# Kernel optimization log

Hardware: AMD Instinct MI355X
Metric: run time of the kernel (lower is better)

Reference implementation:

```python
import jax, jax.numpy as jnp
import numpy as np

NUM_HEADS = 16
HEAD_DIM = 64
D_MODEL = 1024
WINDOW = 256
ROPE_BASE = 10000.0
LN_EPS = 1e-5


def setup_inputs() -> dict:
    key = jax.random.key(0)
    k1, k2, k3, k4 = jax.random.split(key, 4)
    B, S, D = 1, 2048, D_MODEL
    x = jax.random.normal(k1, (B, S, D), dtype=jnp.float32)
    state = jax.random.normal(k2, (B, D), dtype=jnp.float32)
    # nn.Linear(d, 3d, bias=False): y = x @ W_qkv with W_qkv: [D, 3D]
    W_qkv = jax.random.normal(k3, (D, 3 * D), dtype=jnp.float32) / np.sqrt(D)
    W_out = jax.random.normal(k4, (D, D), dtype=jnp.float32) / np.sqrt(D)
    ln_gamma = jnp.ones((D,), dtype=jnp.float32)
    ln_beta = jnp.zeros((D,), dtype=jnp.float32)
    return {"x": x, "state": state, "W_qkv": W_qkv, "W_out": W_out,
            "ln_gamma": ln_gamma, "ln_beta": ln_beta}


def _rotate_half(t):
    h = t.shape[-1] // 2
    return jnp.concatenate([-t[..., h:], t[..., :h]], axis=-1)


def _rope(q, k):
    # q, k: [B, H, S, Hd]
    S, Hd = q.shape[2], q.shape[3]
    inv_freq = 1.0 / (ROPE_BASE ** (jnp.arange(0, Hd, 2, dtype=jnp.float32) / Hd))
    ang = jnp.arange(S, dtype=jnp.float32)[:, None] * inv_freq[None, :]  # [S, Hd/2]
    cos = jnp.concatenate([jnp.cos(ang), jnp.cos(ang)], axis=-1)[None, None]  # [1,1,S,Hd]
    sin = jnp.concatenate([jnp.sin(ang), jnp.sin(ang)], axis=-1)[None, None]
    return q * cos + _rotate_half(q) * sin, k * cos + _rotate_half(k) * sin


def _local_causal_mask(S):
    idx = jnp.arange(S)
    dist = idx[:, None] - idx[None, :]
    allowed = (dist >= 0) & (dist <= WINDOW)
    # Faithful to source: allowed positions get 1.0 (softmax-shift-invariant), else -inf
    return jnp.where(allowed, 1.0, -jnp.inf).astype(jnp.float32)[None, None]


def reference(x, state, W_qkv, W_out, ln_gamma, ln_beta):
    B, S, D = x.shape
    H, Hd = NUM_HEADS, HEAD_DIM
    qkv = (x @ W_qkv).reshape(B, S, 3, H, Hd).transpose(2, 0, 3, 1, 4)  # [3,B,H,S,Hd]
    q, k, v = qkv[0], qkv[1], qkv[2]
    q, k = _rope(q, k)
    scores = jnp.einsum("bhsd,bhtd->bhst", q, k) / np.sqrt(Hd) + _local_causal_mask(S)
    attn = jax.nn.softmax(scores, axis=-1)
    out = jnp.einsum("bhst,bhtd->bhsd", attn, v)  # [B,H,S,Hd]
    out = out.transpose(0, 2, 1, 3).reshape(B, S, D)
    res = x + out @ W_out
    mu = jnp.mean(res, axis=-1, keepdims=True)
    var = jnp.var(res, axis=-1, keepdims=True)
    y = (res - mu) * jax.lax.rsqrt(var + LN_EPS) * ln_gamma + ln_beta
    return y, state
```

## Files before the change

### kernel.cpp

```cpp
#include <hip/hip_runtime.h>
#include <math.h>

#define S_LEN 2048
#define DMODEL 1024
#define NHEADS 16
#define HDIM 64
#define WIN 256
#define N_QKV 3072

typedef __attribute__((ext_vector_type(8))) short s16x8;
typedef __attribute__((ext_vector_type(8))) _Float16 f16x8;
typedef __attribute__((ext_vector_type(4))) _Float16 f16x4;
typedef __attribute__((ext_vector_type(4))) float f32x4;

__device__ inline unsigned short f2bf(float f) {
    unsigned int u = __float_as_uint(f);
    u += 0x7FFFu + ((u >> 16) & 1u);
    return (unsigned short)(u >> 16);
}
__device__ inline float bf2f(unsigned short h) {
    return __uint_as_float(((unsigned int)h) << 16);
}

__global__ __launch_bounds__(256) void cvt_f16(
    const float* __restrict__ src, _Float16* __restrict__ dst)
{
    int i = blockIdx.x * 256 + threadIdx.x;
    float4 v = *(const float4*)&src[i * 4];
    f16x4 o;
    o[0] = (_Float16)v.x; o[1] = (_Float16)v.y;
    o[2] = (_Float16)v.z; o[3] = (_Float16)v.w;
    *(f16x4*)&dst[i * 4] = o;
}

__global__ __launch_bounds__(256) void transpose_cvt(
    const float* __restrict__ W, _Float16* __restrict__ T, int K, int N)
{
    __shared__ float t[32][33];
    const int tx = threadIdx.x & 31;
    const int ty = threadIdx.x >> 5;
    const int n0 = blockIdx.x * 32, k0 = blockIdx.y * 32;

    #pragma unroll
    for (int i = 0; i < 4; ++i)
        t[ty + i * 8][tx] = W[(size_t)(k0 + ty + i * 8) * N + n0 + tx];
    __syncthreads();
    #pragma unroll
    for (int i = 0; i < 4; ++i) {
        int n = n0 + ty + i * 8;
        T[(size_t)n * K + k0 + tx] = (_Float16)t[tx][ty + i * 8];
    }
}

template<int BM, int BN, int WM, int WN, bool RES>
__global__ __launch_bounds__(256) void gemm_f16(
    const _Float16* __restrict__ A, const _Float16* __restrict__ B,
    const float* __restrict__ resid, float* __restrict__ C,
    int M, int N, int K)
{
    constexpr int MI = WM / 16;
    constexpr int NJ = WN / 16;
    constexpr int APASS = BM / 64;
    constexpr int BPASS = BN / 64;
    static_assert(WM * 2 == BM && WN * 2 == BN, "4 waves as 2x2");

    __shared__ _Float16 As[BM * 32];
    __shared__ _Float16 Bs[BN * 32];

    const int tid  = threadIdx.x;
    const int w    = tid >> 6;
    const int lane = tid & 63;
    const int m16  = lane & 15;
    const int g    = lane >> 4;
    const int wr   = w >> 1, wc = w & 1;
    const int bm   = blockIdx.y * BM, bn = blockIdx.x * BN;

    f32x4 acc[MI][NJ];
    #pragma unroll
    for (int i = 0; i < MI; ++i)
        #pragma unroll
        for (int j = 0; j < NJ; ++j) acc[i][j] = (f32x4)(0.0f);

    uint4 ra[APASS], rb[BPASS];

    #pragma unroll
    for (int p = 0; p < APASS; ++p) {
        int f = p * 256 + tid, row = f >> 2, cb = f & 3;
        ra[p] = *(const uint4*)&A[(size_t)(bm + row) * K + cb * 8];
    }
    #pragma unroll
    for (int p = 0; p < BPASS; ++p) {
        int f = p * 256 + tid, row = f >> 2, cb = f & 3;
        rb[p] = *(const uint4*)&B[(size_t)(bn + row) * K + cb * 8];
    }

    const int NT = K / 32;
    for (int kt = 0; kt < NT; ++kt) {
        __syncthreads();
        #pragma unroll
        for (int p = 0; p < APASS; ++p) {
            int f = p * 256 + tid, row = f >> 2, cb = f & 3;
            *(uint4*)&As[row * 32 + ((cb ^ ((row >> 1) & 3)) << 3)] = ra[p];
        }
        #pragma unroll
        for (int p = 0; p < BPASS; ++p) {
            int f = p * 256 + tid, row = f >> 2, cb = f & 3;
            *(uint4*)&Bs[row * 32 + ((cb ^ ((row >> 1) & 3)) << 3)] = rb[p];
        }
        __syncthreads();

        if (kt + 1 < NT) {
            int k0 = (kt + 1) * 32;
            #pragma unroll
            for (int p = 0; p < APASS; ++p) {
                int f = p * 256 + tid, row = f >> 2, cb = f & 3;
                ra[p] = *(const uint4*)&A[(size_t)(bm + row) * K + k0 + cb * 8];
            }
            #pragma unroll
            for (int p = 0; p < BPASS; ++p) {
                int f = p * 256 + tid, row = f >> 2, cb = f & 3;
                rb[p] = *(const uint4*)&B[(size_t)(bn + row) * K + k0 + cb * 8];
            }
        }

        f16x8 af[MI], bf_[NJ];
        #pragma unroll
        for (int i = 0; i < MI; ++i) {
            int row = wr * WM + i * 16 + m16;
            af[i] = *(const f16x8*)&As[row * 32 + ((g ^ ((row >> 1) & 3)) << 3)];
        }
        #pragma unroll
        for (int j = 0; j < NJ; ++j) {
            int row = wc * WN + j * 16 + m16;
            bf_[j] = *(const f16x8*)&Bs[row * 32 + ((g ^ ((row >> 1) & 3)) << 3)];
        }
        #pragma unroll
        for (int j = 0; j < NJ; ++j)
            #pragma unroll
            for (int i = 0; i < MI; ++i)
                acc[i][j] = __builtin_amdgcn_mfma_f32_16x16x32_f16(
                    af[i], bf_[j], acc[i][j], 0, 0, 0);
    }

    const int g4 = g * 4;
    #pragma unroll
    for (int i = 0; i < MI; ++i)
        #pragma unroll
        for (int j = 0; j < NJ; ++j) {
            int col = bn + wc * WN + j * 16 + m16;
            #pragma unroll
            for (int r = 0; r < 4; ++r) {
                int row = bm + wr * WM + i * 16 + g4 + r;
                float val = acc[i][j][r];
                if (RES) val += resid[(size_t)row * N + col];
                C[(size_t)row * N + col] = val;
            }
        }
}

__global__ __launch_bounds__(256) void rope_scatter(
    const float* __restrict__ qkv, float* __restrict__ q,
    unsigned short* __restrict__ khi, unsigned short* __restrict__ klo)
{
    int idx = blockIdx.x * 256 + threadIdx.x;
    int s  = idx >> 10;
    int r  = idx & 1023;
    int hd = r & 63;
    int h  = r >> 6;
    const float* row = qkv + (size_t)s * N_QKV;

    float qv = row[r];
    float kv = row[DMODEL + r];

    int   i   = hd & 31;
    float inv = expf(-(float)i * 0.2878231366242553f);
    float ang = (float)s * inv;
    float c  = cosf(ang);
    float sn = sinf(ang);

    int   pr  = (hd < 32) ? r + 32 : r - 32;
    float sgn = (hd < 32) ? -1.0f : 1.0f;

    float qo = qv * c + sgn * row[pr] * sn;
    float ko = kv * c + sgn * row[DMODEL + pr] * sn;

    size_t o = ((size_t)h * S_LEN + s) * HDIM + hd;
    q[o] = qo;
    unsigned short kh = f2bf(ko);
    khi[o] = kh;
    klo[o] = f2bf(ko - bf2f(kh));
}

__global__ __launch_bounds__(256) void v_transpose(
    const float* __restrict__ qkv, unsigned short* __restrict__ vT)
{
    __shared__ float t[64][65];
    const int s0 = blockIdx.x * 64;
    const int h  = blockIdx.y;
    const int tid = threadIdx.x;
    const int dq  = (tid & 15) * 4;
    const int sl0 = tid >> 4;

    #pragma unroll
    for (int p = 0; p < 4; ++p) {
        int sl = sl0 + p * 16;
        float4 v = *(const float4*)&qkv[(size_t)(s0 + sl) * N_QKV + 2 * DMODEL + h * HDIM + dq];
        t[sl][dq] = v.x; t[sl][dq + 1] = v.y; t[sl][dq + 2] = v.z; t[sl][dq + 3] = v.w;
    }
    __syncthreads();
    #pragma unroll
    for (int p = 0; p < 2; ++p) {
        int u = tid + p * 256;
        int d = u >> 3, sb = (u & 7) * 8;
        s16x8 o;
        #pragma unroll
        for (int i = 0; i < 8; ++i) o[i] = (short)f2bf(t[sb + i][d]);
        *(s16x8*)&vT[((size_t)h * HDIM + d) * S_LEN + s0 + sb] = o;
    }
}

#define KP 72
__global__ __launch_bounds__(256, 3) void attn_mfma(
    const float* __restrict__ qg, const unsigned short* __restrict__ khg,
    const unsigned short* __restrict__ klg, const unsigned short* __restrict__ vTg,
    _Float16* __restrict__ oh)
{
    __shared__ __align__(16) unsigned short Kh[64][KP], Kl[64][KP], Vt[64][KP];
    __shared__ __align__(16) unsigned short Pw[4][16][40];

    const int h   = blockIdx.y;
    const int s0  = blockIdx.x * 64;
    const int tid = threadIdx.x;
    const int w   = tid >> 6, lane = tid & 63;
    const int m16 = lane & 15, g = lane >> 4;
    const int t_base = s0 - 256;

    const int qrow = s0 + w * 16 + m16;
    const float* qp = qg + ((size_t)h * S_LEN + qrow) * HDIM;
    s16x8 qh[2], ql[2];
    #pragma unroll
    for (int c = 0; c < 2; ++c) {
        float4 f0 = *(const float4*)&qp[c * 32 + g * 8];
        float4 f1 = *(const float4*)&qp[c * 32 + g * 8 + 4];
        float f[8] = {f0.x, f0.y, f0.z, f0.w, f1.x, f1.y, f1.z, f1.w};
        #pragma unroll
        for (int j = 0; j < 8; ++j) {
            float v = f[j] * 0.125f;
            unsigned short hb = f2bf(v);
            qh[c][j] = (short)hb;
            ql[c][j] = (short)f2bf(v - bf2f(hb));
        }
    }

    const int qb = w * 16 + m16;
    int lo_b = 256 - s0; if (lo_b < qb) lo_b = qb;
    const int hi_b = qb + 256;

    f32x4 O[4];
    #pragma unroll
    for (int nt = 0; nt < 4; ++nt) O[nt] = (f32x4)(0.0f);
    float l_r[4] = {0.0f, 0.0f, 0.0f, 0.0f};
    float m_col = -1e30f;

    const int stage_min = (s0 >= 256) ? 0 : ((193 - s0 + 63) >> 6);

    for (int st = stage_min; st < 5; ++st) {
        __syncthreads();
        const int t0s = t_base + st * 64;
        #pragma unroll
        for (int pp = 0; pp < 2; ++pp) {
            int u = tid + pp * 256;
            int row = u >> 3, cb = (u & 7) * 8;
            int t = t0s + row;
            s16x8 vh = {}, vl = {};
            if (t >= 0) {
                size_t base = ((size_t)h * S_LEN + t) * HDIM + cb;
                vh = *(const s16x8*)&khg[base];
                vl = *(const s16x8*)&klg[base];
            }
            *(s16x8*)&Kh[row][cb] = vh;
            *(s16x8*)&Kl[row][cb] = vl;
        }
        #pragma unroll
        for (int pp = 0; pp < 2; ++pp) {
            int u = tid + pp * 256;
            int d = u >> 3, kb = (u & 7) * 8;
            int t = t0s + kb;
            s16x8 vv = {};
            if (t >= 0)
                vv = *(const s16x8*)&vTg[((size_t)h * HDIM + d) * S_LEN + t];
            *(s16x8*)&Vt[d][kb] = vv;
        }
        __syncthreads();

        #pragma unroll
        for (int ch = 0; ch < 2; ++ch) {
            f32x4 sc[2];
            #pragma unroll
            for (int kt2 = 0; kt2 < 2; ++kt2) {
                int krow = ch * 32 + kt2 * 16 + m16;
                s16x8 kh0 = *(const s16x8*)&Kh[krow][g * 8];
                s16x8 kh1 = *(const s16x8*)&Kh[krow][32 + g * 8];
                s16x8 kl0 = *(const s16x8*)&Kl[krow][g * 8];
                s16x8 kl1 = *(const s16x8*)&Kl[krow][32 + g * 8];
                f32x4 a = (f32x4)(0.0f);
                a = __builtin_amdgcn_mfma_f32_16x16x32_bf16(kh0, qh[0], a, 0, 0, 0);
                a = __builtin_amdgcn_mfma_f32_16x16x32_bf16(kh1, qh[1], a, 0, 0, 0);
                a = __builtin_amdgcn_mfma_f32_16x16x32_bf16(kh0, ql[0], a, 0, 0, 0);
                a = __builtin_amdgcn_mfma_f32_16x16x32_bf16(kh1, ql[1], a, 0, 0, 0);
                a = __builtin_amdgcn_mfma_f32_16x16x32_bf16(kl0, qh[0], a, 0, 0, 0);
                a = __builtin_amdgcn_mfma_f32_16x16x32_bf16(kl1, qh[1], a, 0, 0, 0);
                sc[kt2] = a;
            }

            float scm[8];
            float pmax = -1e30f;
            #pragma unroll
            for (int kt2 = 0; kt2 < 2; ++kt2)
                #pragma unroll
                for (int r = 0; r < 4; ++r) {
                    int ki = st * 64 + ch * 32 + kt2 * 16 + 4 * g + r;
                    bool vd = (ki >= lo_b) && (ki <= hi_b);
                    float s_ = vd ? sc[kt2][r] : -1e30f;
                    scm[kt2 * 4 + r] = s_;
                    pmax = fmaxf(pmax, s_);
                }
            pmax = fmaxf(pmax, __shfl_xor(pmax, 16));
            pmax = fmaxf(pmax, __shfl_xor(pmax, 32));
            float mnew = fmaxf(m_col, pmax);

            float p[8];
            float psum = 0.0f;
            #pragma unroll
            for (int i = 0; i < 8; ++i) {
                float e = (scm[i] > -9e29f) ? __expf(scm[i] - mnew) : 0.0f;
                p[i] = e;
                psum += e;
            }
            psum += __shfl_xor(psum, 16);
            psum += __shfl_xor(psum, 32);
            float scale = __expf(m_col - mnew);
            m_col = mnew;

            #pragma unroll
            for (int r = 0; r < 4; ++r) {
                float sr = __shfl(scale, 4 * g + r);
                float ps = __shfl(psum, 4 * g + r);
                l_r[r] = l_r[r] * sr + ps;
                O[0][r] *= sr; O[1][r] *= sr; O[2][r] *= sr; O[3][r] *= sr;
            }

            unsigned int d0, d1, d2, d3;
            asm("v_cvt_pk_bf16_f32 %0, %1, %2" : "=v"(d0) : "v"(p[0]), "v"(p[1]));
            asm("v_cvt_pk_bf16_f32 %0, %1, %2" : "=v"(d1) : "v"(p[2]), "v"(p[3]));
            asm("v_cvt_pk_bf16_f32 %0, %1, %2" : "=v"(d2) : "v"(p[4]), "v"(p[5]));
            asm("v_cvt_pk_bf16_f32 %0, %1, %2" : "=v"(d3) : "v"(p[6]), "v"(p[7]));
            *(uint2*)&Pw[w][m16][4 * g]      = make_uint2(d0, d1);
            *(uint2*)&Pw[w][m16][16 + 4 * g] = make_uint2(d2, d3);
            asm volatile("s_waitcnt lgkmcnt(0)" ::: "memory");
            __builtin_amdgcn_sched_barrier(0);
            s16x8 pa = *(const s16x8*)&Pw[w][m16][g * 8];

            #pragma unroll
            for (int nt = 0; nt < 4; ++nt) {
                s16x8 vb = *(const s16x8*)&Vt[nt * 16 + m16][ch * 32 + g * 8];
                O[nt] = __builtin_amdgcn_mfma_f32_16x16x32_bf16(pa, vb, O[nt], 0, 0, 0);
            }
        }
    }

    #pragma unroll
    for (int r = 0; r < 4; ++r) {
        float linv = 1.0f / l_r[r];
        int srow = s0 + w * 16 + 4 * g + r;
        size_t obase = (size_t)srow * DMODEL + h * HDIM;
        #pragma unroll
        for (int nt = 0; nt < 4; ++nt)
            oh[obase + nt * 16 + m16] = (_Float16)(O[nt][r] * linv);
    }
}

__global__ __launch_bounds__(256) void layernorm_k(
    const float* __restrict__ res, const float* __restrict__ gamma,
    const float* __restrict__ beta, float* __restrict__ y)
{
    const int row  = blockIdx.x;
    const int tid  = threadIdx.x;
    const int wave = tid >> 6;
    const int lane = tid & 63;
    const float* r = res + (size_t)row * DMODEL;

    float4 xv = *(const float4*)&r[tid * 4];
    float ssum = xv.x + xv.y + xv.z + xv.w;
    float ssq  = xv.x * xv.x + xv.y * xv.y + xv.z * xv.z + xv.w * xv.w;

    #pragma unroll
    for (int off = 1; off < 64; off <<= 1) {
        ssum += __shfl_xor(ssum, off);
        ssq  += __shfl_xor(ssq, off);
    }

    __shared__ float wsum[4], wsq[4];
    if (lane == 0) { wsum[wave] = ssum; wsq[wave] = ssq; }
    __syncthreads();

    float tot  = wsum[0] + wsum[1] + wsum[2] + wsum[3];
    float tot2 = wsq[0] + wsq[1] + wsq[2] + wsq[3];
    float mu   = tot * (1.0f / DMODEL);
    float var  = tot2 * (1.0f / DMODEL) - mu * mu;
    float rstd = rsqrtf(var + 1e-5f);

    float4 gm = *(const float4*)&gamma[tid * 4];
    float4 be = *(const float4*)&beta[tid * 4];
    float4 yo;
    yo.x = (xv.x - mu) * rstd * gm.x + be.x;
    yo.y = (xv.y - mu) * rstd * gm.y + be.y;
    yo.z = (xv.z - mu) * rstd * gm.z + be.z;
    yo.w = (xv.w - mu) * rstd * gm.w + be.w;
    *(float4*)&y[(size_t)row * DMODEL + tid * 4] = yo;
}

extern "C" void kernel_launch(void* const* d_in, const int* in_sizes, int n_in,
                              void* d_out, int out_size, void* d_ws, size_t ws_size,
                              hipStream_t stream) {
    const float* x     = (const float*)d_in[0];
    const float* state = (const float*)d_in[1];
    const float* Wqkv  = (const float*)d_in[2];
    const float* Wout  = (const float*)d_in[3];
    const float* gamma = (const float*)d_in[4];
    const float* beta  = (const float*)d_in[5];
    float* out = (float*)d_out;

    char* base = (char*)d_ws;
    float*     qkv_raw = (float*)base;
    _Float16*  ah      = (_Float16*)base;
    float*     res     = (float*)(base + 8388608);
    float*          qb  = (float*)(base + 25165824);
    unsigned short* khi = (unsigned short*)(base + 33554432);
    unsigned short* klo = (unsigned short*)(base + 37748736);
    unsigned short* vT  = (unsigned short*)(base + 41943040);
    _Float16* WqkvT = (_Float16*)(base + 46137344);
    _Float16* WoutT = (_Float16*)(base + 52428800);
    _Float16* xh    = (_Float16*)(base + 54525952);

    cvt_f16<<<(S_LEN * DMODEL) / 1024, 256, 0, stream>>>(x, xh);
    transpose_cvt<<<dim3(N_QKV / 32, DMODEL / 32), 256, 0, stream>>>(
        Wqkv, WqkvT, DMODEL, N_QKV);
    transpose_cvt<<<dim3(DMODEL / 32, DMODEL / 32), 256, 0, stream>>>(
        Wout, WoutT, DMODEL, DMODEL);

    gemm_f16<128, 64, 64, 32, false>
        <<<dim3(N_QKV / 64, S_LEN / 128), 256, 0, stream>>>(
            xh, WqkvT, nullptr, qkv_raw, S_LEN, N_QKV, DMODEL);

    rope_scatter<<<(S_LEN * DMODEL) / 256, 256, 0, stream>>>(qkv_raw, qb, khi, klo);

    v_transpose<<<dim3(S_LEN / 64, NHEADS), 256, 0, stream>>>(qkv_raw, vT);

    attn_mfma<<<dim3(S_LEN / 64, NHEADS), 256, 0, stream>>>(
        qb, khi, klo, vT, ah);

    gemm_f16<64, 64, 32, 32, true>
        <<<dim3(DMODEL / 64, S_LEN / 64), 256, 0, stream>>>(
            ah, WoutT, x, res, S_LEN, DMODEL, DMODEL);

    layernorm_k<<<S_LEN, 256, 0, stream>>>(res, gamma, beta, out);

    hipMemcpyAsync(out + (size_t)S_LEN * DMODEL, state,
                   (size_t)DMODEL * sizeof(float),
                   hipMemcpyDeviceToDevice, stream);
}
```

Baseline: 185.1 us.

## Use fp16 single-pass QK, direct-to-LDS GEMM loads, precomputed RoPE table

Replaces the split-bf16 (hi/lo) three-term QK^T product with a single fp16 MFMA pass, folding the 1/sqrt(d) scale into RoPE and storing q and k as fp16. The GEMMs switch from register-staged double buffering to global_load_lds direct loads with a new swizzle, and the QKV GEMM tile grows to 128x128. RoPE cos/sin values are precomputed into a table by a separate kernel instead of being evaluated per element. These changes cut QK MFMA work, memory traffic and transcendental math. The costs are reduced precision in the scores and the loss of prefetch overlap in the GEMM main loop.

```diff
diff --git a/kernel.cpp b/kernel.cpp
--- a/kernel.cpp
+++ b/kernel.cpp
@@ -13,6 +13,9 @@
 typedef __attribute__((ext_vector_type(4))) _Float16 f16x4;
 typedef __attribute__((ext_vector_type(4))) float f32x4;
 
+typedef __attribute__((address_space(1))) const void gas_void;
+typedef __attribute__((address_space(3))) void las_void;
+
 __device__ inline unsigned short f2bf(float f) {
     unsigned int u = __float_as_uint(f);
     u += 0x7FFFu + ((u >> 16) & 1u);
@@ -33,6 +36,15 @@
     *(f16x4*)&dst[i * 4] = o;
 }
 
+__global__ __launch_bounds__(256) void rope_tab_k(float2* __restrict__ tab)
+{
+    int idx = blockIdx.x * 256 + threadIdx.x;
+    int s = idx >> 5, i = idx & 31;
+    float inv = expf(-(float)i * 0.2878231366242553f);
+    float ang = (float)s * inv;
+    tab[idx] = make_float2(cosf(ang), sinf(ang));
+}
+
 __global__ __launch_bounds__(256) void transpose_cvt(
     const float* __restrict__ W, _Float16* __restrict__ T, int K, int N)
 {
@@ -52,28 +64,26 @@
     }
 }
 
-template<int BM, int BN, int WM, int WN, bool RES>
-__global__ __launch_bounds__(256) void gemm_f16(
+template<int BM, int BN, bool RES>
+__global__ __launch_bounds__(256) void gemm_lds(
     const _Float16* __restrict__ A, const _Float16* __restrict__ B,
     const float* __restrict__ resid, float* __restrict__ C,
     int M, int N, int K)
 {
-    constexpr int MI = WM / 16;
-    constexpr int NJ = WN / 16;
-    constexpr int APASS = BM / 64;
-    constexpr int BPASS = BN / 64;
-    static_assert(WM * 2 == BM && WN * 2 == BN, "4 waves as 2x2");
+    constexpr int WM = BM / 2, WN = BN / 2;
+    constexpr int MI = WM / 16, NJ = WN / 16;
 
     __shared__ _Float16 As[BM * 32];
     __shared__ _Float16 Bs[BN * 32];
 
-    const int tid  = threadIdx.x;
-    const int w    = tid >> 6;
-    const int lane = tid & 63;
-    const int m16  = lane & 15;
-    const int g    = lane >> 4;
-    const int wr   = w >> 1, wc = w & 1;
-    const int bm   = blockIdx.y * BM, bn = blockIdx.x * BN;
+    const int tid = threadIdx.x;
+    const int w = tid >> 6, lane = tid & 63;
+    const int m16 = lane & 15, g = lane >> 4;
+    const int wr = w >> 1, wc = w & 1;
+    const int bm = blockIdx.y * BM, bn = blockIdx.x * BN;
+
+    const int srow = lane >> 2;
+    const int sgran = (lane & 3) ^ (srow & 3);
 
     f32x4 acc[MI][NJ];
     #pragma unroll
@@ -81,58 +91,35 @@
         #pragma unroll
         for (int j = 0; j < NJ; ++j) acc[i][j] = (f32x4)(0.0f);
 
-    uint4 ra[APASS], rb[BPASS];
-
-    #pragma unroll
-    for (int p = 0; p < APASS; ++p) {
-        int f = p * 256 + tid, row = f >> 2, cb = f & 3;
-        ra[p] = *(const uint4*)&A[(size_t)(bm + row) * K + cb * 8];
-    }
-    #pragma unroll
-    for (int p = 0; p < BPASS; ++p) {
-        int f = p * 256 + tid, row = f >> 2, cb = f & 3;
-        rb[p] = *(const uint4*)&B[(size_t)(bn + row) * K + cb * 8];
-    }
-
-    const int NT = K / 32;
-    for (int kt = 0; kt < NT; ++kt) {
+    for (int kt = 0; kt < K / 32; ++kt) {
+        const int k0 = kt * 32;
         __syncthreads();
         #pragma unroll
-        for (int p = 0; p < APASS; ++p) {
-            int f = p * 256 + tid, row = f >> 2, cb = f & 3;
-            *(uint4*)&As[row * 32 + ((cb ^ ((row >> 1) & 3)) << 3)] = ra[p];
-        }
-        #pragma unroll
-        for (int p = 0; p < BPASS; ++p) {
-            int f = p * 256 + tid, row = f >> 2, cb = f & 3;
-            *(uint4*)&Bs[row * 32 + ((cb ^ ((row >> 1) & 3)) << 3)] = rb[p];
+        for (int p = 0; p < BM / 64; ++p) {
+            int row = p * 64 + w * 16 + srow;
+            __builtin_amdgcn_global_load_lds(
+                (gas_void*)&A[(size_t)(bm + row) * K + k0 + sgran * 8],
+                (las_void*)&As[(p * 64 + w * 16) * 32], 16, 0, 0);
+        }
+        #pragma unroll
+        for (int p = 0; p < BN / 64; ++p) {
+            int row = p * 64 + w * 16 + srow;
+            __builtin_amdgcn_global_load_lds(
+                (gas_void*)&B[(size_t)(bn + row) * K + k0 + sgran * 8],
+                (las_void*)&Bs[(p * 64 + w * 16) * 32], 16, 0, 0);
         }
         __syncthreads();
-
-        if (kt + 1 < NT) {
-            int k0 = (kt + 1) * 32;
-            #pragma unroll
-            for (int p = 0; p < APASS; ++p) {
-                int f = p * 256 + tid, row = f >> 2, cb = f & 3;
-                ra[p] = *(const uint4*)&A[(size_t)(bm + row) * K + k0 + cb * 8];
-            }
-            #pragma unroll
-            for (int p = 0; p < BPASS; ++p) {
-                int f = p * 256 + tid, row = f >> 2, cb = f & 3;
-                rb[p] = *(const uint4*)&B[(size_t)(bn + row) * K + k0 + cb * 8];
-            }
-        }
 
         f16x8 af[MI], bf_[NJ];
         #pragma unroll
         for (int i = 0; i < MI; ++i) {
             int row = wr * WM + i * 16 + m16;
-            af[i] = *(const f16x8*)&As[row * 32 + ((g ^ ((row >> 1) & 3)) << 3)];
+            af[i] = *(const f16x8*)&As[row * 32 + ((g ^ (row & 3)) << 3)];
         }
         #pragma unroll
         for (int j = 0; j < NJ; ++j) {
             int row = wc * WN + j * 16 + m16;
-            bf_[j] = *(const f16x8*)&Bs[row * 32 + ((g ^ ((row >> 1) & 3)) << 3)];
+            bf_[j] = *(const f16x8*)&Bs[row * 32 + ((g ^ (row & 3)) << 3)];
         }
         #pragma unroll
         for (int j = 0; j < NJ; ++j)
@@ -159,8 +146,8 @@
 }
 
 __global__ __launch_bounds__(256) void rope_scatter(
-    const float* __restrict__ qkv, float* __restrict__ q,
-    unsigned short* __restrict__ khi, unsigned short* __restrict__ klo)
+    const float* __restrict__ qkv, const float2* __restrict__ tab,
+    _Float16* __restrict__ qf, _Float16* __restrict__ kf)
 {
     int idx = blockIdx.x * 256 + threadIdx.x;
     int s  = idx >> 10;
@@ -172,23 +159,16 @@
     float qv = row[r];
     float kv = row[DMODEL + r];
 
-    int   i   = hd & 31;
-    float inv = expf(-(float)i * 0.2878231366242553f);
-    float ang = (float)s * inv;
-    float c  = cosf(ang);
-    float sn = sinf(ang);
-
+    float2 cs = tab[s * 32 + (hd & 31)];
     int   pr  = (hd < 32) ? r + 32 : r - 32;
     float sgn = (hd < 32) ? -1.0f : 1.0f;
 
-    float qo = qv * c + sgn * row[pr] * sn;
-    float ko = kv * c + sgn * row[DMODEL + pr] * sn;
+    float qo = (qv * cs.x + sgn * row[pr] * cs.y) * 0.125f;
+    float ko =  kv * cs.x + sgn * row[DMODEL + pr] * cs.y;
 
     size_t o = ((size_t)h * S_LEN + s) * HDIM + hd;
-    q[o] = qo;
-    unsigned short kh = f2bf(ko);
-    khi[o] = kh;
-    klo[o] = f2bf(ko - bf2f(kh));
+    qf[o] = (_Float16)qo;
+    kf[o] = (_Float16)ko;
 }
 
 __global__ __launch_bounds__(256) void v_transpose(
@@ -221,11 +201,11 @@
 
 #define KP 72
 __global__ __launch_bounds__(256, 3) void attn_mfma(
-    const float* __restrict__ qg, const unsigned short* __restrict__ khg,
-    const unsigned short* __restrict__ klg, const unsigned short* __restrict__ vTg,
-    _Float16* __restrict__ oh)
-{
-    __shared__ __align__(16) unsigned short Kh[64][KP], Kl[64][KP], Vt[64][KP];
+    const _Float16* __restrict__ qg, const _Float16* __restrict__ kg,
+    const unsigned short* __restrict__ vTg, _Float16* __restrict__ oh)
+{
+    __shared__ __align__(16) _Float16 Ks[64][KP];
+    __shared__ __align__(16) unsigned short Vt[64][KP];
     __shared__ __align__(16) unsigned short Pw[4][16][40];
 
     const int h   = blockIdx.y;
@@ -236,25 +216,14 @@
     const int t_base = s0 - 256;
 
     const int qrow = s0 + w * 16 + m16;
-    const float* qp = qg + ((size_t)h * S_LEN + qrow) * HDIM;
-    s16x8 qh[2], ql[2];
-    #pragma unroll
-    for (int c = 0; c < 2; ++c) {
-        float4 f0 = *(const float4*)&qp[c * 32 + g * 8];
-        float4 f1 = *(const float4*)&qp[c * 32 + g * 8 + 4];
-        float f[8] = {f0.x, f0.y, f0.z, f0.w, f1.x, f1.y, f1.z, f1.w};
-        #pragma unroll
-        for (int j = 0; j < 8; ++j) {
-            float v = f[j] * 0.125f;
-            unsigned short hb = f2bf(v);
-            qh[c][j] = (short)hb;
-            ql[c][j] = (short)f2bf(v - bf2f(hb));
-        }
-    }
-
-    const int qb = w * 16 + m16;
-    int lo_b = 256 - s0; if (lo_b < qb) lo_b = qb;
-    const int hi_b = qb + 256;
+    const _Float16* qp = qg + ((size_t)h * S_LEN + qrow) * HDIM;
+    f16x8 qf[2];
+    qf[0] = *(const f16x8*)&qp[g * 8];
+    qf[1] = *(const f16x8*)&qp[32 + g * 8];
+
+    const int qb_ = w * 16 + m16;
+    int lo_b = 256 - s0; if (lo_b < qb_) lo_b = qb_;
+    const int hi_b = qb_ + 256;
 
     f32x4 O[4];
     #pragma unroll
@@ -272,14 +241,10 @@
             int u = tid + pp * 256;
             int row = u >> 3, cb = (u & 7) * 8;
             int t = t0s + row;
-            s16x8 vh = {}, vl = {};
-            if (t >= 0) {
-                size_t base = ((size_t)h * S_LEN + t) * HDIM + cb;
-                vh = *(const s16x8*)&khg[base];
-                vl = *(const s16x8*)&klg[base];
-            }
-            *(s16x8*)&Kh[row][cb] = vh;
-            *(s16x8*)&Kl[row][cb] = vl;
+            f16x8 kv = {};
+            if (t >= 0)
+                kv = *(const f16x8*)&kg[((size_t)h * S_LEN + t) * HDIM + cb];
+            *(f16x8*)&Ks[row][cb] = kv;
         }
         #pragma unroll
         for (int pp = 0; pp < 2; ++pp) {
@@ -299,17 +264,11 @@
             #pragma unroll
             for (int kt2 = 0; kt2 < 2; ++kt2) {
                 int krow = ch * 32 + kt2 * 16 + m16;
-                s16x8 kh0 = *(const s16x8*)&Kh[krow][g * 8];
-                s16x8 kh1 = *(const s16x8*)&Kh[krow][32 + g * 8];
-                s16x8 kl0 = *(const s16x8*)&Kl[krow][g * 8];
-                s16x8 kl1 = *(const s16x8*)&Kl[krow][32 + g * 8];
+                f16x8 k0 = *(const f16x8*)&Ks[krow][g * 8];
+                f16x8 k1 = *(const f16x8*)&Ks[krow][32 + g * 8];
                 f32x4 a = (f32x4)(0.0f);
-                a = __builtin_amdgcn_mfma_f32_16x16x32_bf16(kh0, qh[0], a, 0, 0, 0);
-                a = __builtin_amdgcn_mfma_f32_16x16x32_bf16(kh1, qh[1], a, 0, 0, 0);
-                a = __builtin_amdgcn_mfma_f32_16x16x32_bf16(kh0, ql[0], a, 0, 0, 0);
-                a = __builtin_amdgcn_mfma_f32_16x16x32_bf16(kh1, ql[1], a, 0, 0, 0);
-                a = __builtin_amdgcn_mfma_f32_16x16x32_bf16(kl0, qh[0], a, 0, 0, 0);
-                a = __builtin_amdgcn_mfma_f32_16x16x32_bf16(kl1, qh[1], a, 0, 0, 0);
+                a = __builtin_amdgcn_mfma_f32_16x16x32_f16(k0, qf[0], a, 0, 0, 0);
+                a = __builtin_amdgcn_mfma_f32_16x16x32_f16(k1, qf[1], a, 0, 0, 0);
                 sc[kt2] = a;
             }
 
@@ -435,32 +394,33 @@
     float*     qkv_raw = (float*)base;
     _Float16*  ah      = (_Float16*)base;
     float*     res     = (float*)(base + 8388608);
-    float*          qb  = (float*)(base + 25165824);
-    unsigned short* khi = (unsigned short*)(base + 33554432);
-    unsigned short* klo = (unsigned short*)(base + 37748736);
-    unsigned short* vT  = (unsigned short*)(base + 41943040);
-    _Float16* WqkvT = (_Float16*)(base + 46137344);
-    _Float16* WoutT = (_Float16*)(base + 52428800);
-    _Float16* xh    = (_Float16*)(base + 54525952);
+    _Float16*  qf      = (_Float16*)(base + 25165824);
+    _Float16*  kf      = (_Float16*)(base + 29360128);
+    unsigned short* vT = (unsigned short*)(base + 33554432);
+    _Float16*  WqkvT   = (_Float16*)(base + 37748736);
+    _Float16*  WoutT   = (_Float16*)(base + 44040192);
+    _Float16*  xh      = (_Float16*)(base + 46137344);
+    float2*    tab     = (float2*)(base + 50331648);
 
     cvt_f16<<<(S_LEN * DMODEL) / 1024, 256, 0, stream>>>(x, xh);
+    rope_tab_k<<<(S_LEN * 32) / 256, 256, 0, stream>>>(tab);
     transpose_cvt<<<dim3(N_QKV / 32, DMODEL / 32), 256, 0, stream>>>(
         Wqkv, WqkvT, DMODEL, N_QKV);
     transpose_cvt<<<dim3(DMODEL / 32, DMODEL / 32), 256, 0, stream>>>(
         Wout, WoutT, DMODEL, DMODEL);
 
-    gemm_f16<128, 64, 64, 32, false>
-        <<<dim3(N_QKV / 64, S_LEN / 128), 256, 0, stream>>>(
+    gemm_lds<128, 128, false>
+        <<<dim3(N_QKV / 128, S_LEN / 128), 256, 0, stream>>>(
             xh, WqkvT, nullptr, qkv_raw, S_LEN, N_QKV, DMODEL);
 
-    rope_scatter<<<(S_LEN * DMODEL) / 256, 256, 0, stream>>>(qkv_raw, qb, khi, klo);
+    rope_scatter<<<(S_LEN * DMODEL) / 256, 256, 0, stream>>>(
+        qkv_raw, tab, qf, kf);
 
     v_transpose<<<dim3(S_LEN / 64, NHEADS), 256, 0, stream>>>(qkv_raw, vT);
 
-    attn_mfma<<<dim3(S_LEN / 64, NHEADS), 256, 0, stream>>>(
-        qb, khi, klo, vT, ah);
-
-    gemm_f16<64, 64, 32, 32, true>
+    attn_mfma<<<dim3(S_LEN / 64, NHEADS), 256, 0, stream>>>(qf, kf, vT, ah);
+
+    gemm_lds<64, 64, true>
         <<<dim3(DMODEL / 64, S_LEN / 64), 256, 0, stream>>>(
             ah, WoutT, x, res, S_LEN, DMODEL, DMODEL);
 
```

Result: faster. 161.6 us (-12.7%).
